# Kernel optimization log

Hardware: AMD Instinct MI355X
Metric: run time of the kernel (lower is better)

Reference implementation:

```python
import jax, jax.numpy as jnp
import numpy as np

N, F_IN, HID, HEADS, E, G, CLS = 20000, 128, 32, 8, 320000, 64, 10


def setup_inputs() -> dict:
    key = jax.random.key(0)
    ks = jax.random.split(key, 16)
    HC = HEADS * HID
    inp = {
        'x': jax.random.normal(ks[0], (N, F_IN), jnp.float32),
        'edge_index': jax.random.randint(ks[1], (2, E), 0, N, jnp.int64),
        'batch': jnp.sort(jax.random.randint(ks[2], (N,), 0, G, jnp.int64)),
        'W1': jax.random.normal(ks[3], (F_IN, HC), jnp.float32) * 0.1,
        'att_l1': jax.random.normal(ks[4], (HEADS, HID), jnp.float32) * 0.1,
        'att_r1': jax.random.normal(ks[5], (HEADS, HID), jnp.float32) * 0.1,
        'b1': jnp.zeros((HC,), jnp.float32),
        'W2': jax.random.normal(ks[6], (HC, HC), jnp.float32) * 0.1,
        'att_l2': jax.random.normal(ks[7], (HEADS, HID), jnp.float32) * 0.1,
        'att_r2': jax.random.normal(ks[8], (HEADS, HID), jnp.float32) * 0.1,
        'b2': jnp.zeros((HC,), jnp.float32),
        'lin_W': jax.random.normal(ks[9], (HC, CLS), jnp.float32) * 0.1,
        'lin_b': jnp.zeros((CLS,), jnp.float32),
    }
    return inp


def _add_self_loops(edge_index):
    loops = jnp.arange(N, dtype=edge_index.dtype)
    return (jnp.concatenate([edge_index[0], loops]),
            jnp.concatenate([edge_index[1], loops]))


def _supergat_conv(x, edge_index, W, att_l, att_r, b):
    # SuperGATConv, attention_type='MX', eval mode (no dropout / neg sampling)
    h = (x @ W).reshape(-1, HEADS, HID)          # [N, H, C]
    src, dst = _add_self_loops(edge_index)       # j -> i
    x_j = h[src]                                 # [Etot, H, C]
    x_i = h[dst]
    logits = jnp.einsum('ehc,ehc->eh', x_i, x_j)            # dot-product part
    alpha = jnp.einsum('ehc,hc->eh', x_j, att_l) + jnp.einsum('ehc,hc->eh', x_i, att_r)
    alpha = alpha * jax.nn.sigmoid(logits)
    alpha = jax.nn.leaky_relu(alpha, 0.2)
    # segment softmax over incoming edges of each dst node
    amax = jax.ops.segment_max(alpha, dst, num_segments=N)
    ex = jnp.exp(alpha - amax[dst])
    denom = jax.ops.segment_sum(ex, dst, num_segments=N)
    attn = ex / (denom[dst] + 1e-16)             # [Etot, H]
    out = jax.ops.segment_sum(x_j * attn[..., None], dst, num_segments=N)  # [N,H,C]
    return out.reshape(-1, HEADS * HID) + b


def reference(x, edge_index, batch, W1, att_l1, att_r1, b1, W2, att_l2, att_r2, b2, lin_W, lin_b):
    h = _supergat_conv(x, edge_index, W1, att_l1, att_r1, b1)
    h = jax.nn.elu(h)
    h = _supergat_conv(h, edge_index, W2, att_l2, att_r2, b2)
    # global mean pool over graphs
    sums = jax.ops.segment_sum(h, batch, num_segments=G)
    cnts = jax.ops.segment_sum(jnp.ones((h.shape[0], 1), h.dtype), batch, num_segments=G)
    pooled = sums / jnp.maximum(cnts, 1.0)
    return pooled @ lin_W + lin_b
```

## Files before the change

kernel.cpp:

```cpp
#include <hip/hip_runtime.h>
#include <hip/hip_bf16.h>
#include <math.h>

#define NNODE 20000
#define FIN   128
#define HC    256
#define HEADS 8
#define HID   32
#define NEDGE 320000
#define ETOT  (NEDGE + NNODE)
#define NGRAPH 64
#define NCLS  10
#define MAXDEG 64

typedef __attribute__((ext_vector_type(8))) short short8v;
typedef __attribute__((ext_vector_type(8))) unsigned short ushort8v;
typedef __attribute__((ext_vector_type(4))) float float4v;

__device__ __forceinline__ ushort f2bf(float f) {
    __hip_bfloat16 b = __float2bfloat16(f);
    return *(ushort*)&b;
}
__device__ __forceinline__ float bf2f(ushort u) {
    return __uint_as_float(((unsigned)u) << 16);
}


#define ZB_DEG ((NNODE + 255) / 256)
#define ZB_PS  ((NGRAPH * HC + NGRAPH + 255) / 256)

__global__ __launch_bounds__(256) void init_kernel(const float* __restrict__ W1,
                                                   const float* __restrict__ W2,
                                                   ushort* __restrict__ W1t,
                                                   ushort* __restrict__ W2t,
                                                   int* __restrict__ deg,
                                                   float* __restrict__ psum) {
    int b = blockIdx.x;
    if (b < 128) {
        int e = b * 256 + threadIdx.x;
        int k = e >> 8, n = e & 255;
        W1t[(long)n * FIN + k] = f2bf(W1[(long)k * 256 + n]);
    } else if (b < 384) {
        int e = (b - 128) * 256 + threadIdx.x;
        int k = e >> 8, n = e & 255;
        W2t[(long)n * HC + k] = f2bf(W2[(long)k * 256 + n]);
    } else if (b < 384 + ZB_DEG) {
        int i = (b - 384) * 256 + threadIdx.x;
        if (i < NNODE) deg[i] = 0;
    } else {
        int i = (b - 384 - ZB_DEG) * 256 + threadIdx.x;
        if (i < NGRAPH * HC + NGRAPH) psum[i] = 0.f;
    }
}


__global__ __launch_bounds__(256) void fill_slots(const int* __restrict__ ei,
                                                  int* __restrict__ deg,
                                                  int* __restrict__ esrc) {
    int e = blockIdx.x * blockDim.x + threadIdx.x;
    if (e >= ETOT) return;
    int src, dst;
    if (e < NEDGE) { src = ei[e]; dst = ei[NEDGE + e]; }
    else           { src = e - NEDGE; dst = src; }
    int slot = atomicAdd(&deg[dst], 1);
    if (slot < MAXDEG) esrc[dst * MAXDEG + slot] = src;
}


template<bool A_FP32>
__global__ __launch_bounds__(256) void gemm_mfma(const void* __restrict__ Aptr,
                                                 const ushort* __restrict__ Bt,
                                                 ushort* __restrict__ C,
                                                 const float* __restrict__ attL,
                                                 const float* __restrict__ attR,
                                                 float* __restrict__ aL,
                                                 float* __restrict__ aR,
                                                 int M, int K) {
    __shared__ __align__(16) ushort As[64][72];
    __shared__ __align__(16) ushort Bs[64][72];
    int tid = threadIdx.x;
    int rowBase = blockIdx.x * 64;
    int colBase = blockIdx.y * 64;
    int wave = tid >> 6;
    int l = tid & 63;
    int lm = l & 15;
    int quad = l >> 4;
    int r0 = (wave >> 1) * 32;
    int c0 = (wave & 1) * 32;

    float4v acc00 = {0.f, 0.f, 0.f, 0.f};
    float4v acc01 = acc00, acc10 = acc00, acc11 = acc00;

    for (int k0 = 0; k0 < K; k0 += 64) {
        if (A_FP32) {
            const float* A = (const float*)Aptr;
            #pragma unroll
            for (int q = 0; q < 4; q++) {
                int idx = tid + q * 256;
                int r   = idx >> 4;
                int kc  = (idx & 15) * 4;
                int grow = rowBase + r;
                float4 v = make_float4(0.f, 0.f, 0.f, 0.f);
                if (grow < M) v = *(const float4*)(A + (long)grow * K + k0 + kc);
                ushort4 o = { f2bf(v.x), f2bf(v.y), f2bf(v.z), f2bf(v.w) };
                *(ushort4*)&As[r][kc] = o;
            }
            #pragma unroll
            for (int q = 0; q < 2; q++) {
                int ch = tid + q * 256;
                int r  = ch >> 3;
                int kc = (ch & 7) * 8;
                *(short8v*)&Bs[r][kc] =
                    *(const short8v*)(Bt + (long)(colBase + r) * K + k0 + kc);
            }
        } else {
            const ushort* A = (const ushort*)Aptr;
            #pragma unroll
            for (int q = 0; q < 2; q++) {
                int ch = tid + q * 256;
                int r  = ch >> 3;
                int kc = (ch & 7) * 8;
                int grow = rowBase + r;
                short8v av = {};
                if (grow < M) av = *(const short8v*)(A + (long)grow * K + k0 + kc);
                *(short8v*)&As[r][kc] = av;
                *(short8v*)&Bs[r][kc] =
                    *(const short8v*)(Bt + (long)(colBase + r) * K + k0 + kc);
            }
        }
        __syncthreads();
        #pragma unroll
        for (int ks = 0; ks < 64; ks += 32) {
            int kb = ks + quad * 8;
            short8v a0 = *(const short8v*)&As[r0 + lm][kb];
            short8v a1 = *(const short8v*)&As[r0 + 16 + lm][kb];
            short8v b0 = *(const short8v*)&Bs[c0 + lm][kb];
            short8v b1 = *(const short8v*)&Bs[c0 + 16 + lm][kb];
            acc00 = __builtin_amdgcn_mfma_f32_16x16x32_bf16(a0, b0, acc00, 0, 0, 0);
            acc01 = __builtin_amdgcn_mfma_f32_16x16x32_bf16(a0, b1, acc01, 0, 0, 0);
            acc10 = __builtin_amdgcn_mfma_f32_16x16x32_bf16(a1, b0, acc10, 0, 0, 0);
            acc11 = __builtin_amdgcn_mfma_f32_16x16x32_bf16(a1, b1, acc11, 0, 0, 0);
        }
        __syncthreads();
    }

    int cb = colBase + c0;
    int hd = cb >> 5;
    float al0 = attL[cb + lm], al1 = attL[cb + 16 + lm];
    float ar0 = attR[cb + lm], ar1 = attR[cb + 16 + lm];
    #pragma unroll
    for (int mi = 0; mi < 2; mi++) {
        float4v s0 = mi ? acc10 : acc00;
        float4v s1 = mi ? acc11 : acc01;
        #pragma unroll
        for (int r = 0; r < 4; r++) {
            int row = rowBase + r0 + mi * 16 + quad * 4 + r;
            float pl = s0[r] * al0 + s1[r] * al1;
            float pr = s0[r] * ar0 + s1[r] * ar1;
            #pragma unroll
            for (int s2 = 1; s2 < 16; s2 <<= 1) {
                pl += __shfl_xor(pl, s2);
                pr += __shfl_xor(pr, s2);
            }
            if (row < M) {
                C[(long)row * 256 + cb + lm]      = f2bf(s0[r]);
                C[(long)row * 256 + cb + 16 + lm] = f2bf(s1[r]);
                if (lm == 0) {
                    aL[row * 8 + hd] = pl;
                    aR[row * 8 + hd] = pr;
                }
            }
        }
    }
}


__global__ __launch_bounds__(256) void fused_attn(const ushort* __restrict__ h,
                                                  const int* __restrict__ degv,
                                                  const int* __restrict__ esrc,
                                                  const float* __restrict__ aL,
                                                  const float* __restrict__ aR,
                                                  const float* __restrict__ bias,
                                                  ushort* __restrict__ out,
                                                  int apply_elu) {
    int wave = threadIdx.x >> 6;
    int node = blockIdx.x * 4 + wave;
    if (node >= NNODE) return;
    int l = threadIdx.x & 63;
    int slot = l >> 5;
    int lh = l & 31;
    int head = lh >> 2;

    const ushort8v* h8 = (const ushort8v*)h;
    ushort8v hiu = h8[(long)node * 32 + lh];
    float hi[8];
    #pragma unroll
    for (int c = 0; c < 8; c++) hi[c] = bf2f(hiu[c]);
    float a_ri = aR[node * 8 + head];
    int beg = node * MAXDEG;
    int deg = min(degv[node], MAXDEG);

    float lsum = 0.f;
    float acc[8] = {0.f, 0.f, 0.f, 0.f, 0.f, 0.f, 0.f, 0.f};

    int p  = slot;
    int j  = (p < deg)     ? esrc[beg + p]     : 0;
    int jn = (p + 2 < deg) ? esrc[beg + p + 2] : 0;
    for (; p < deg; p += 2) {
        ushort8v hju = h8[(long)j * 32 + lh];
        float a_lj = aL[j * 8 + head];
        j = jn;
        jn = (p + 4 < deg) ? esrc[beg + p + 4] : 0;
        float hj[8];
        #pragma unroll
        for (int c = 0; c < 8; c++) hj[c] = bf2f(hju[c]);
        float prod = hi[0] * hj[0];
        #pragma unroll
        for (int c = 1; c < 8; c++) prod += hi[c] * hj[c];
        prod += __shfl_xor(prod, 1);
        prod += __shfl_xor(prod, 2);
        float alpha = (a_lj + a_ri) * __builtin_amdgcn_rcpf(1.f + __expf(-prod));
        alpha = (alpha > 0.f) ? alpha : 0.2f * alpha;
        float ex = __expf(alpha);
        lsum += ex;
        #pragma unroll
        for (int c = 0; c < 8; c++) acc[c] += ex * hj[c];
    }

    lsum += __shfl_xor(lsum, 32);
    #pragma unroll
    for (int c = 0; c < 8; c++) acc[c] += __shfl_xor(acc[c], 32);

    if (slot == 0) {
        float inv = __builtin_amdgcn_rcpf(lsum + 1e-16f);
        float4 b0 = ((const float4*)bias)[lh * 2];
        float4 b1 = ((const float4*)bias)[lh * 2 + 1];
        float bb[8] = {b0.x, b0.y, b0.z, b0.w, b1.x, b1.y, b1.z, b1.w};
        ushort8v o;
        #pragma unroll
        for (int c = 0; c < 8; c++) {
            float r = acc[c] * inv + bb[c];
            if (apply_elu) r = (r > 0.f) ? r : (__expf(r) - 1.f);
            o[c] = f2bf(r);
        }
        *(ushort8v*)(out + (long)node * 256 + lh * 8) = o;
    }
}


__global__ __launch_bounds__(256) void pool_kernel(const ushort* __restrict__ h,
                                                   const int* __restrict__ batch,
                                                   float* __restrict__ psum,
                                                   float* __restrict__ pcnt) {
    int t = threadIdx.x;
    int n0 = blockIdx.x * 64;
    int n1 = min(n0 + 64, NNODE);
    if (n0 >= NNODE) return;
    float accv = 0.f;
    int gcur = batch[n0];
    for (int n = n0; n < n1; ++n) {
        int g = batch[n];
        if (g != gcur) {
            atomicAdd(&psum[gcur * HC + t], accv);
            accv = 0.f;
            gcur = g;
        }
        accv += bf2f(h[(long)n * HC + t]);
    }
    atomicAdd(&psum[gcur * HC + t], accv);
    if (t == 0) {
        int cnt = 0;
        int gc = batch[n0];
        for (int n = n0; n < n1; ++n) {
            int g = batch[n];
            if (g != gc) { atomicAdd(&pcnt[gc], (float)cnt); cnt = 0; gc = g; }
            cnt++;
        }
        atomicAdd(&pcnt[gc], (float)cnt);
    }
}

__global__ void final_kernel(const float* __restrict__ psum, const float* __restrict__ pcnt,
                             const float* __restrict__ linW, const float* __restrict__ linb,
                             float* __restrict__ out) {
    int g = blockIdx.x;
    int t = threadIdx.x;
    __shared__ float p[HC];
    float c = fmaxf(pcnt[g], 1.f);
    p[t] = psum[g * HC + t] / c;
    __syncthreads();
    if (t < NCLS) {
        float s = linb[t];
        for (int cch = 0; cch < HC; cch++) s += p[cch] * linW[cch * NCLS + t];
        out[g * NCLS + t] = s;
    }
}


extern "C" void kernel_launch(void* const* d_in, const int* in_sizes, int n_in,
                              void* d_out, int out_size, void* d_ws, size_t ws_size,
                              hipStream_t stream) {
    const float* x     = (const float*)d_in[0];
    const int*   ei    = (const int*)d_in[1];
    const int*   batch = (const int*)d_in[2];
    const float* W1    = (const float*)d_in[3];
    const float* attL1 = (const float*)d_in[4];
    const float* attR1 = (const float*)d_in[5];
    const float* b1    = (const float*)d_in[6];
    const float* W2    = (const float*)d_in[7];
    const float* attL2 = (const float*)d_in[8];
    const float* attR2 = (const float*)d_in[9];
    const float* b2    = (const float*)d_in[10];
    const float* linW  = (const float*)d_in[11];
    const float* linb  = (const float*)d_in[12];
    float* out = (float*)d_out;

    char* w = (char*)d_ws;
    size_t o = 0;
    int* deg    = (int*)(w + o); o += (size_t)NNODE * 4;
    o = (o + 15) & ~(size_t)15;
    int* esrc   = (int*)(w + o); o += (size_t)NNODE * MAXDEG * 4;
    o = (o + 15) & ~(size_t)15;
    ushort* W1t = (ushort*)(w + o); o += (size_t)FIN * HC * 2;
    ushort* W2t = (ushort*)(w + o); o += (size_t)HC * HC * 2;
    o = (o + 15) & ~(size_t)15;
    ushort* hbA = (ushort*)(w + o); o += (size_t)NNODE * HC * 2;
    ushort* hbB = (ushort*)(w + o); o += (size_t)NNODE * HC * 2;
    o = (o + 15) & ~(size_t)15;
    float* aL   = (float*)(w + o); o += (size_t)NNODE * HEADS * 4;
    float* aR   = (float*)(w + o); o += (size_t)NNODE * HEADS * 4;
    float* psum = (float*)(w + o); o += (size_t)NGRAPH * HC * 4;
    float* pcnt = (float*)(w + o); o += (size_t)NGRAPH * 4;

    init_kernel<<<384 + ZB_DEG + ZB_PS, 256, 0, stream>>>(W1, W2, W1t, W2t, deg, psum);

    int eb = (ETOT + 255) / 256;
    fill_slots<<<eb, 256, 0, stream>>>(ei, deg, esrc);

    dim3 gg((NNODE + 63) / 64, HC / 64);
    int ab = (NNODE + 3) / 4;
    gemm_mfma<true><<<gg, 256, 0, stream>>>(x, W1t, hbA, attL1, attR1, aL, aR, NNODE, FIN);
    fused_attn<<<ab, 256, 0, stream>>>(hbA, deg, esrc, aL, aR, b1, hbB, 1);
    gemm_mfma<false><<<gg, 256, 0, stream>>>(hbB, W2t, hbA, attL2, attR2, aL, aR, NNODE, HC);
    fused_attn<<<ab, 256, 0, stream>>>(hbA, deg, esrc, aL, aR, b2, hbB, 0);
    pool_kernel<<<(NNODE + 63) / 64, 256, 0, stream>>>(hbB, batch, psum, pcnt);
    final_kernel<<<NGRAPH, 256, 0, stream>>>(psum, pcnt, linW, linb, out);
}
```

Measured before the change: 218.9 us.

## Merge edge slot filling into first GEMM launch and prefetch neighbor rows

The separate fill_slots launch is folded into the first GEMM kernel as extra blocks, so the atomic edge bucketing runs alongside the layer-1 GEMM in one launch instead of two serialized ones. In fused_attn, the neighbor feature row and its aL value are now loaded one iteration ahead (software pipelining), which hides gather latency at the cost of more live registers. The fill blocks and GEMM blocks now share a grid, so the LDS allocation of the GEMM body also applies to the fill blocks and may reduce their occupancy.

```diff
diff --git a/kernel.cpp b/kernel.cpp
--- a/kernel.cpp
+++ b/kernel.cpp
@@ -12,6 +12,9 @@
 #define NGRAPH 64
 #define NCLS  10
 #define MAXDEG 64
+
+#define GEMM1_BLKS (((NNODE + 63) / 64) * 4)
+#define FILL_BLKS  ((ETOT + 255) / 256)
 
 typedef __attribute__((ext_vector_type(8))) short short8v;
 typedef __attribute__((ext_vector_type(8))) unsigned short ushort8v;
@@ -54,33 +57,20 @@
 }
 
 
-__global__ __launch_bounds__(256) void fill_slots(const int* __restrict__ ei,
-                                                  int* __restrict__ deg,
-                                                  int* __restrict__ esrc) {
-    int e = blockIdx.x * blockDim.x + threadIdx.x;
-    if (e >= ETOT) return;
-    int src, dst;
-    if (e < NEDGE) { src = ei[e]; dst = ei[NEDGE + e]; }
-    else           { src = e - NEDGE; dst = src; }
-    int slot = atomicAdd(&deg[dst], 1);
-    if (slot < MAXDEG) esrc[dst * MAXDEG + slot] = src;
-}
-
-
 template<bool A_FP32>
-__global__ __launch_bounds__(256) void gemm_mfma(const void* __restrict__ Aptr,
-                                                 const ushort* __restrict__ Bt,
-                                                 ushort* __restrict__ C,
-                                                 const float* __restrict__ attL,
-                                                 const float* __restrict__ attR,
-                                                 float* __restrict__ aL,
-                                                 float* __restrict__ aR,
-                                                 int M, int K) {
+__device__ __forceinline__ void gemm_body(const void* __restrict__ Aptr,
+                                          const ushort* __restrict__ Bt,
+                                          ushort* __restrict__ C,
+                                          const float* __restrict__ attL,
+                                          const float* __restrict__ attR,
+                                          float* __restrict__ aL,
+                                          float* __restrict__ aR,
+                                          int M, int K, int rowBlk, int colBlk) {
     __shared__ __align__(16) ushort As[64][72];
     __shared__ __align__(16) ushort Bs[64][72];
     int tid = threadIdx.x;
-    int rowBase = blockIdx.x * 64;
-    int colBase = blockIdx.y * 64;
+    int rowBase = rowBlk * 64;
+    int colBase = colBlk * 64;
     int wave = tid >> 6;
     int l = tid & 63;
     int lm = l & 15;
@@ -172,6 +162,42 @@
             }
         }
     }
+}
+
+
+__global__ __launch_bounds__(256) void gemm1_fill(const float* __restrict__ x,
+                                                  const ushort* __restrict__ W1t,
+                                                  ushort* __restrict__ C,
+                                                  const float* __restrict__ attL,
+                                                  const float* __restrict__ attR,
+                                                  float* __restrict__ aL,
+                                                  float* __restrict__ aR,
+                                                  const int* __restrict__ ei,
+                                                  int* __restrict__ deg,
+                                                  int* __restrict__ esrc) {
+    if (blockIdx.x < GEMM1_BLKS) {
+        gemm_body<true>(x, W1t, C, attL, attR, aL, aR, NNODE, FIN,
+                        blockIdx.x >> 2, blockIdx.x & 3);
+    } else {
+        int e = (blockIdx.x - GEMM1_BLKS) * 256 + threadIdx.x;
+        if (e < ETOT) {
+            int src, dst;
+            if (e < NEDGE) { src = ei[e]; dst = ei[NEDGE + e]; }
+            else           { src = e - NEDGE; dst = src; }
+            int slot = atomicAdd(&deg[dst], 1);
+            if (slot < MAXDEG) esrc[dst * MAXDEG + slot] = src;
+        }
+    }
+}
+
+__global__ __launch_bounds__(256) void gemm2_kernel(const ushort* __restrict__ A,
+                                                    const ushort* __restrict__ Bt,
+                                                    ushort* __restrict__ C,
+                                                    const float* __restrict__ attL,
+                                                    const float* __restrict__ attR,
+                                                    float* __restrict__ aL,
+                                                    float* __restrict__ aR) {
+    gemm_body<false>(A, Bt, C, attL, attR, aL, aR, NNODE, HC, blockIdx.x, blockIdx.y);
 }
 
 
@@ -203,28 +229,33 @@
     float lsum = 0.f;
     float acc[8] = {0.f, 0.f, 0.f, 0.f, 0.f, 0.f, 0.f, 0.f};
 
-    int p  = slot;
-    int j  = (p < deg)     ? esrc[beg + p]     : 0;
-    int jn = (p + 2 < deg) ? esrc[beg + p + 2] : 0;
+    int p = slot;
+    int j0 = (p < deg) ? esrc[beg + p] : 0;
+    ushort8v hjA = h8[(long)j0 * 32 + lh];
+    float alA = aL[j0 * 8 + head];
+    int j1 = (p + 2 < deg) ? esrc[beg + p + 2] : 0;
+
     for (; p < deg; p += 2) {
-        ushort8v hju = h8[(long)j * 32 + lh];
-        float a_lj = aL[j * 8 + head];
-        j = jn;
-        jn = (p + 4 < deg) ? esrc[beg + p + 4] : 0;
+        ushort8v hjB = h8[(long)j1 * 32 + lh];
+        float alB = aL[j1 * 8 + head];
+        int j2 = (p + 4 < deg) ? esrc[beg + p + 4] : 0;
+
         float hj[8];
         #pragma unroll
-        for (int c = 0; c < 8; c++) hj[c] = bf2f(hju[c]);
+        for (int c = 0; c < 8; c++) hj[c] = bf2f(hjA[c]);
         float prod = hi[0] * hj[0];
         #pragma unroll
         for (int c = 1; c < 8; c++) prod += hi[c] * hj[c];
         prod += __shfl_xor(prod, 1);
         prod += __shfl_xor(prod, 2);
-        float alpha = (a_lj + a_ri) * __builtin_amdgcn_rcpf(1.f + __expf(-prod));
+        float alpha = (alA + a_ri) * __builtin_amdgcn_rcpf(1.f + __expf(-prod));
         alpha = (alpha > 0.f) ? alpha : 0.2f * alpha;
         float ex = __expf(alpha);
         lsum += ex;
         #pragma unroll
         for (int c = 0; c < 8; c++) acc[c] += ex * hj[c];
+
+        hjA = hjB; alA = alB; j1 = j2;
     }
 
     lsum += __shfl_xor(lsum, 32);
@@ -334,14 +365,12 @@
 
     init_kernel<<<384 + ZB_DEG + ZB_PS, 256, 0, stream>>>(W1, W2, W1t, W2t, deg, psum);
 
-    int eb = (ETOT + 255) / 256;
-    fill_slots<<<eb, 256, 0, stream>>>(ei, deg, esrc);
-
+    int ab = (NNODE + 3) / 4;
+    gemm1_fill<<<GEMM1_BLKS + FILL_BLKS, 256, 0, stream>>>(
+        x, W1t, hbA, attL1, attR1, aL, aR, ei, deg, esrc);
+    fused_attn<<<ab, 256, 0, stream>>>(hbA, deg, esrc, aL, aR, b1, hbB, 1);
     dim3 gg((NNODE + 63) / 64, HC / 64);
-    int ab = (NNODE + 3) / 4;
-    gemm_mfma<true><<<gg, 256, 0, stream>>>(x, W1t, hbA, attL1, attR1, aL, aR, NNODE, FIN);
-    fused_attn<<<ab, 256, 0, stream>>>(hbA, deg, esrc, aL, aR, b1, hbB, 1);
-    gemm_mfma<false><<<gg, 256, 0, stream>>>(hbB, W2t, hbA, attL2, attR2, aL, aR, NNODE, HC);
+    gemm2_kernel<<<gg, 256, 0, stream>>>(hbB, W2t, hbA, attL2, attR2, aL, aR);
     fused_attn<<<ab, 256, 0, stream>>>(hbA, deg, esrc, aL, aR, b2, hbB, 0);
     pool_kernel<<<(NNODE + 63) / 64, 256, 0, stream>>>(hbB, batch, psum, pcnt);
     final_kernel<<<NGRAPH, 256, 0, stream>>>(psum, pcnt, linW, linb, out);
```

After: 223.8 us. 2.2% more time.
